# Kernel optimization log

Hardware: AMD Instinct MI355X
Metric: run time of the kernel (lower is better)

## Reference

```python
import jax, jax.numpy as jnp
import numpy as np

N_HEAD, D_K, D_V, EPS = 8, 64, 64, 1e-6


def setup_inputs() -> dict:
    key = jax.random.key(0)
    ks = jax.random.split(key, 7)
    b, n, t, d = 8, 4, 512, 512
    q = jax.random.normal(ks[0], (b, n, t, d), dtype=jnp.float32)
    k = jax.random.normal(ks[1], (b, n, t, d), dtype=jnp.float32)
    v = jax.random.normal(ks[2], (b, n, t, d), dtype=jnp.float32)
    s = 1.0 / np.sqrt(d)
    w_q = jax.random.normal(ks[3], (N_HEAD * D_K, d), dtype=jnp.float32) * s
    w_k = jax.random.normal(ks[4], (N_HEAD * D_K, d), dtype=jnp.float32) * s
    w_v = jax.random.normal(ks[5], (N_HEAD * D_V, d), dtype=jnp.float32) * s
    w_fc = jax.random.normal(ks[6], (d, N_HEAD * D_V), dtype=jnp.float32) * s
    ln_gamma = jnp.ones((d,), dtype=jnp.float32)
    ln_beta = jnp.zeros((d,), dtype=jnp.float32)
    return {"q": q, "k": k, "v": v, "w_q": w_q, "w_k": w_k, "w_v": w_v,
            "w_fc": w_fc, "ln_gamma": ln_gamma, "ln_beta": ln_beta}


def reference(q, k, v, w_q, w_k, w_v, w_fc, ln_gamma, ln_beta):
    b, n, t, d = q.shape
    B = b * n
    qf = q.reshape(B, t, d)
    kf = k.reshape(B, t, d)
    vf = v.reshape(B, t, d)
    residual = qf
    # projections -> [B, H, T, dk/dv]
    Q = jnp.einsum('btd,ed->bte', qf, w_q).reshape(B, t, N_HEAD, D_K).transpose(0, 2, 1, 3)
    K = jnp.einsum('btd,ed->bte', kf, w_k).reshape(B, t, N_HEAD, D_K).transpose(0, 2, 1, 3)
    V = jnp.einsum('btd,ed->bte', vf, w_v).reshape(B, t, N_HEAD, D_V).transpose(0, 2, 1, 3)
    # scaled dot-product attention (scale by sqrt(d_k) of q's last dim)
    scale = 1.0 / jnp.sqrt(jnp.asarray(D_K, dtype=Q.dtype))
    attn = jax.nn.softmax(jnp.einsum('bhqd,bhkd->bhqk', Q * scale, K), axis=-1)
    O = jnp.einsum('bhqk,bhkd->bhqd', attn, V)  # [B, H, T, dv]
    # merge heads, then the original's extra transpose+view (layout scramble)
    x = O.transpose(0, 2, 1, 3).reshape(B, t, N_HEAD * D_V)
    x = jnp.transpose(x, (0, 2, 1)).reshape(B, t, N_HEAD * D_V)
    x = jnp.einsum('bte,de->btd', x, w_fc)
    x = x + residual
    # LayerNorm(eps=1e-6)
    mu = jnp.mean(x, axis=-1, keepdims=True)
    var = jnp.var(x, axis=-1, keepdims=True)
    x = (x - mu) * jax.lax.rsqrt(var + EPS) * ln_gamma + ln_beta
    return x.reshape(b, n, t, d)
```

## Files before the change

kernel.cpp:

```cpp
#include <hip/hip_runtime.h>
#include <hip/hip_bf16.h>
#include <stdint.h>

typedef __attribute__((ext_vector_type(8))) short bf16x8;
typedef __attribute__((ext_vector_type(4))) float f32x4;
typedef unsigned int u32;

#define MFMA16(a,b,c) __builtin_amdgcn_mfma_f32_16x16x32_bf16((a),(b),(c),0,0,0)

__device__ __forceinline__ unsigned short f2bf(float f) {
    unsigned u = __float_as_uint(f);
    u = (u + 0x7FFFu + ((u >> 16) & 1u)) >> 16;
    return (unsigned short)u;
}
__device__ __forceinline__ float bf2f(unsigned short h) {
    return __uint_as_float(((unsigned)h) << 16);
}
__device__ __forceinline__ void gload16(const unsigned short* gp, unsigned short* lp) {
    __builtin_amdgcn_global_load_lds(
        (const __attribute__((address_space(1))) u32*)gp,
        (__attribute__((address_space(3))) u32*)lp, 16, 0, 0);
}
__device__ __forceinline__ int xcd_swz(int bid, int q8) {
    return (bid & 7) * q8 + (bid >> 3);
}


__global__ __launch_bounds__(256) void prep_kernel(
    const float* __restrict__ q, const float* __restrict__ k, const float* __restrict__ v,
    const float* __restrict__ wq, const float* __restrict__ wk, const float* __restrict__ wv,
    const float* __restrict__ wfc,
    unsigned short* __restrict__ Xq, unsigned short* __restrict__ Xk, unsigned short* __restrict__ Xv,
    unsigned short* __restrict__ Wcat)
{
    const long c = (long)blockIdx.x * 256 + threadIdx.x;
    const float* src;
    unsigned short* dst;
    long off;
    if (c < 3145728) {
        const int t = (int)(c >> 20);
        off = (c & 1048575) * 8;
        src = (t == 0) ? q : (t == 1) ? k : v;
        dst = (t == 0) ? Xq : (t == 1) ? Xk : Xv;
    } else {
        const long c2 = c - 3145728;
        const int w = (int)(c2 >> 15);
        off = (c2 & 32767) * 8;
        src = (w == 0) ? wq : (w == 1) ? wk : (w == 2) ? wv : wfc;
        dst = Wcat + (long)w * 262144;
    }
    const float4 a = *(const float4*)(src + off);
    const float4 b = *(const float4*)(src + off + 4);
    uint4 pk;
    pk.x = (u32)f2bf(a.x) | ((u32)f2bf(a.y) << 16);
    pk.y = (u32)f2bf(a.z) | ((u32)f2bf(a.w) << 16);
    pk.z = (u32)f2bf(b.x) | ((u32)f2bf(b.y) << 16);
    pk.w = (u32)f2bf(b.z) | ((u32)f2bf(b.w) << 16);
    *(uint4*)(dst + off) = pk;
}

__device__ __forceinline__ void gemm_body(
    const unsigned short* __restrict__ A, const unsigned short* __restrict__ Bm,
    unsigned short* __restrict__ out, int mode, float scale,
    unsigned short* As0, unsigned short* Bs0,
    unsigned short* As1, unsigned short* Bs1,
    int m0, int n0)
{
    const int tid = threadIdx.x, wid = tid >> 6, lane = tid & 63;
    const int wm = wid >> 1, wn = wid & 1;
    const int g = lane >> 4, cc = lane & 15;

    f32x4 acc[4][4];
    #pragma unroll
    for (int a = 0; a < 4; a++)
        #pragma unroll
        for (int b = 0; b < 4; b++)
            acc[a][b] = (f32x4){0.f, 0.f, 0.f, 0.f};

    auto STAGE = [&](unsigned short* As, unsigned short* Bs, int k0) {
        #pragma unroll
        for (int j = 0; j < 4; j++) {
            const int sb = j * 256 + wid * 64;
            const int s = sb + lane;
            const int r = s >> 3;
            const int cd = (s & 7) ^ (r & 7);
            gload16(A  + (size_t)(m0 + r) * 512 + k0 + cd * 8, As + (size_t)sb * 8);
            gload16(Bm + (size_t)(n0 + r) * 512 + k0 + cd * 8, Bs + (size_t)sb * 8);
        }
    };

    STAGE(As0, Bs0, 0);
    __syncthreads();

    #pragma unroll
    for (int t = 0; t < 8; t++) {
        unsigned short* Ac = (t & 1) ? As1 : As0;
        unsigned short* Bc = (t & 1) ? Bs1 : Bs0;
        if (t < 7)
            STAGE((t & 1) ? As0 : As1, (t & 1) ? Bs0 : Bs1, (t + 1) * 64);

        #pragma unroll
        for (int kc = 0; kc < 2; kc++) {
            bf16x8 af[4], bfr[4];
            #pragma unroll
            for (int mf = 0; mf < 4; mf++) {
                const int r = wm * 64 + mf * 16 + cc;
                af[mf] = *(const bf16x8*)(Ac + r * 64 + (((kc * 4 + g) ^ (r & 7)) * 8));
            }
            #pragma unroll
            for (int nf = 0; nf < 4; nf++) {
                const int r = wn * 64 + nf * 16 + cc;
                bfr[nf] = *(const bf16x8*)(Bc + r * 64 + (((kc * 4 + g) ^ (r & 7)) * 8));
            }
            __builtin_amdgcn_s_setprio(1);
            #pragma unroll
            for (int mf = 0; mf < 4; mf++)
                #pragma unroll
                for (int nf = 0; nf < 4; nf++)
                    acc[mf][nf] = MFMA16(af[mf], bfr[nf], acc[mf][nf]);
            __builtin_amdgcn_s_setprio(0);
        }
        __syncthreads();
    }

    #pragma unroll
    for (int mf = 0; mf < 4; mf++) {
        const int rg = m0 + wm * 64 + mf * 16 + g * 4;
        const int t0 = rg & 511, bI = rg >> 9;
        #pragma unroll
        for (int nf = 0; nf < 4; nf++) {
            const int col = n0 + wn * 64 + nf * 16 + cc;
            if (mode == 0) {
                const int h = col >> 6, dd = col & 63;
                const size_t base = ((size_t)((bI * 8 + h) * 512 + t0)) * 64 + dd;
                #pragma unroll
                for (int i = 0; i < 4; i++)
                    out[base + (size_t)i * 64] = f2bf(acc[mf][nf][i] * scale);
            } else if (mode == 1) {
                const int h = col >> 6, dd = col & 63;
                const size_t base = ((size_t)((bI * 8 + h) * 64 + dd)) * 512 + t0;
                uint2 pk;
                pk.x = (u32)f2bf(acc[mf][nf][0]) | ((u32)f2bf(acc[mf][nf][1]) << 16);
                pk.y = (u32)f2bf(acc[mf][nf][2]) | ((u32)f2bf(acc[mf][nf][3]) << 16);
                *(uint2*)(out + base) = pk;
            } else {
                #pragma unroll
                for (int i = 0; i < 4; i++)
                    out[(size_t)(rg + i) * 512 + col] = f2bf(acc[mf][nf][i]);
            }
        }
    }
}

__global__ __launch_bounds__(256) void proj_kernel(
    const unsigned short* __restrict__ Xq, const unsigned short* __restrict__ Xk,
    const unsigned short* __restrict__ Xv, const unsigned short* __restrict__ Wcat,
    unsigned short* __restrict__ Qb, unsigned short* __restrict__ Kb,
    unsigned short* __restrict__ Vt)
{
    __shared__ __align__(16) unsigned short As[2][128 * 64];
    __shared__ __align__(16) unsigned short Bs[2][128 * 64];
    const int work = xcd_swz(blockIdx.x, 192);
    const int x = work & 3, y = (work >> 2) & 127, z = work >> 9;
    const unsigned short* A = (z == 0) ? Xq : (z == 1) ? Xk : Xv;
    const unsigned short* B = Wcat + (size_t)z * 262144;
    unsigned short* out = (z == 0) ? Qb : (z == 1) ? Kb : Vt;
    const int mode = (z == 2) ? 1 : 0;
    const float scale = (z == 0) ? 0.125f : 1.0f;
    gemm_body(A, B, out, mode, scale, As[0], Bs[0], As[1], Bs[1], y * 128, x * 128);
}

__global__ __launch_bounds__(256) void fc_kernel(
    const unsigned short* __restrict__ Os, const unsigned short* __restrict__ Wfc,
    unsigned short* __restrict__ Y)
{
    __shared__ __align__(16) unsigned short As[2][128 * 64];
    __shared__ __align__(16) unsigned short Bs[2][128 * 64];
    const int work = xcd_swz(blockIdx.x, 64);
    const int x = work & 3, y = work >> 2;
    gemm_body(Os, Wfc, Y, 2, 1.0f, As[0], Bs[0], As[1], Bs[1], y * 128, x * 128);
}

__global__ __launch_bounds__(256) void attn_kernel(
    const unsigned short* __restrict__ Qb, const unsigned short* __restrict__ Kb,
    const unsigned short* __restrict__ Vt, unsigned short* __restrict__ Os)
{
    __shared__ __align__(16) unsigned short Ks[64 * 64];
    __shared__ __align__(16) unsigned short Vs[64 * 64];
    __shared__ __align__(16) unsigned short Ps[4 * 32 * 64];

    const int work = xcd_swz(blockIdx.x, 128);
    const int qt = work & 3, bh = work >> 2;
    const int tid = threadIdx.x;
    const int wid = tid >> 6, lane = tid & 63;
    const int g = lane >> 4, cc = lane & 15;

    const unsigned short* Qp = Qb + (size_t)bh * 512 * 64;
    const unsigned short* Kp = Kb + (size_t)bh * 512 * 64;
    const unsigned short* Vp = Vt + (size_t)bh * 64 * 512;

    const int q0 = qt * 128 + wid * 32;

    bf16x8 qf[2][2];
    #pragma unroll
    for (int mf = 0; mf < 2; mf++)
        #pragma unroll
        for (int kb = 0; kb < 2; kb++)
            qf[mf][kb] = *(const bf16x8*)(Qp + (size_t)(q0 + mf * 16 + cc) * 64 + kb * 32 + g * 8);

    f32x4 o[2][4];
    #pragma unroll
    for (int a = 0; a < 2; a++)
        #pragma unroll
        for (int b = 0; b < 4; b++)
            o[a][b] = (f32x4){0.f, 0.f, 0.f, 0.f};
    float lrun[2][4];
    #pragma unroll
    for (int a = 0; a < 2; a++)
        #pragma unroll
        for (int i = 0; i < 4; i++) lrun[a][i] = 0.f;

    const int sb = wid * 64;
    const int s1 = sb + lane, r1 = s1 >> 3, cd1 = (s1 & 7) ^ (r1 & 7);
    const int s2 = sb + 256 + lane, r2 = s2 >> 3, cd2 = (s2 & 7) ^ (r2 & 7);

    for (int kt = 0; kt < 8; kt++) {
        gload16(Kp + (size_t)(kt * 64 + r1) * 64 + cd1 * 8, Ks + (size_t)sb * 8);
        gload16(Kp + (size_t)(kt * 64 + r2) * 64 + cd2 * 8, Ks + (size_t)(sb + 256) * 8);
        gload16(Vp + (size_t)r1 * 512 + kt * 64 + cd1 * 8, Vs + (size_t)sb * 8);
        gload16(Vp + (size_t)r2 * 512 + kt * 64 + cd2 * 8, Vs + (size_t)(sb + 256) * 8);
        __syncthreads();

        f32x4 s[2][4];
        #pragma unroll
        for (int a = 0; a < 2; a++)
            #pragma unroll
            for (int b = 0; b < 4; b++)
                s[a][b] = (f32x4){0.f, 0.f, 0.f, 0.f};
        __builtin_amdgcn_s_setprio(1);
        #pragma unroll
        for (int nf = 0; nf < 4; nf++) {
            const int r = nf * 16 + cc;
            #pragma unroll
            for (int kb = 0; kb < 2; kb++) {
                bf16x8 kf = *(const bf16x8*)(Ks + r * 64 + (((kb * 4 + g) ^ (r & 7)) * 8));
                s[0][nf] = MFMA16(qf[0][kb], kf, s[0][nf]);
                s[1][nf] = MFMA16(qf[1][kb], kf, s[1][nf]);
            }
        }
        __builtin_amdgcn_s_setprio(0);

        unsigned short* Pw = Ps + wid * 32 * 64;
        #pragma unroll
        for (int mf = 0; mf < 2; mf++)
            #pragma unroll
            for (int i = 0; i < 4; i++) {
                float lacc = 0.f;
                #pragma unroll
                for (int nf = 0; nf < 4; nf++) {
                    float p = __expf(s[mf][nf][i]);
                    s[mf][nf][i] = p;
                    lacc += p;
                }
                lrun[mf][i] += lacc;
            }

        #pragma unroll
        for (int mf = 0; mf < 2; mf++)
            #pragma unroll
            for (int nf = 0; nf < 4; nf++) {
                const int c = nf * 16 + cc, csl = c >> 3, cin = c & 7;
                #pragma unroll
                for (int i = 0; i < 4; i++) {
                    const int row = mf * 16 + g * 4 + i;
                    Pw[row * 64 + ((csl ^ (row & 7)) * 8) + cin] = f2bf(s[mf][nf][i]);
                }
            }

        __builtin_amdgcn_s_setprio(1);
        #pragma unroll
        for (int kc = 0; kc < 2; kc++) {
            bf16x8 pa[2], vb[4];
            #pragma unroll
            for (int mf = 0; mf < 2; mf++) {
                const int r = mf * 16 + cc;
                pa[mf] = *(const bf16x8*)(Pw + r * 64 + (((kc * 4 + g) ^ (r & 7)) * 8));
            }
            #pragma unroll
            for (int vf = 0; vf < 4; vf++) {
                const int r = vf * 16 + cc;
                vb[vf] = *(const bf16x8*)(Vs + r * 64 + (((kc * 4 + g) ^ (r & 7)) * 8));
            }
            #pragma unroll
            for (int mf = 0; mf < 2; mf++)
                #pragma unroll
                for (int vf = 0; vf < 4; vf++)
                    o[mf][vf] = MFMA16(pa[mf], vb[vf], o[mf][vf]);
        }
        __builtin_amdgcn_s_setprio(0);
        __syncthreads();
    }

    const int b = bh >> 3, h = bh & 7;
    #pragma unroll
    for (int mf = 0; mf < 2; mf++) {
        int tq0 = q0 + mf * 16 + g * 4;
        float inv[4];
        #pragma unroll
        for (int i = 0; i < 4; i++) {
            float l = lrun[mf][i];
            #pragma unroll
            for (int d = 1; d < 16; d <<= 1) l += __shfl_xor(l, d);
            inv[i] = 1.0f / l;
        }
        #pragma unroll
        for (int vf = 0; vf < 4; vf++) {
            int dv = vf * 16 + cc;
            uint2 pk;
            pk.x = (u32)f2bf(o[mf][vf][0] * inv[0]) | ((u32)f2bf(o[mf][vf][1] * inv[1]) << 16);
            pk.y = (u32)f2bf(o[mf][vf][2] * inv[2]) | ((u32)f2bf(o[mf][vf][3] * inv[3]) << 16);
            size_t base = ((size_t)b * 512 + h * 64 + dv) * 512 + tq0;
            *(uint2*)(Os + base) = pk;
        }
    }
}

__global__ __launch_bounds__(256) void ln_kernel(
    const unsigned short* __restrict__ y, const float* __restrict__ resid,
    const float* __restrict__ gamma, const float* __restrict__ beta,
    float* __restrict__ out)
{
    const int wid = threadIdx.x >> 6, lane = threadIdx.x & 63;
    const int row = blockIdx.x * 4 + wid;
    const unsigned short* yr = y + (size_t)row * 512;
    const float* rr = resid + (size_t)row * 512;

    const bf16x8 yv = *(const bf16x8*)(yr + lane * 8);
    const float4 r0 = *(const float4*)(rr + lane * 8);
    const float4 r1 = *(const float4*)(rr + lane * 8 + 4);
    float x[8];
    x[0] = bf2f((unsigned short)yv[0]) + r0.x;
    x[1] = bf2f((unsigned short)yv[1]) + r0.y;
    x[2] = bf2f((unsigned short)yv[2]) + r0.z;
    x[3] = bf2f((unsigned short)yv[3]) + r0.w;
    x[4] = bf2f((unsigned short)yv[4]) + r1.x;
    x[5] = bf2f((unsigned short)yv[5]) + r1.y;
    x[6] = bf2f((unsigned short)yv[6]) + r1.z;
    x[7] = bf2f((unsigned short)yv[7]) + r1.w;

    float s = 0.f, sq = 0.f;
    #pragma unroll
    for (int j = 0; j < 8; j++) { s += x[j]; sq += x[j] * x[j]; }
    #pragma unroll
    for (int d = 1; d < 64; d <<= 1) {
        s += __shfl_xor(s, d);
        sq += __shfl_xor(sq, d);
    }
    const float mu = s * (1.0f / 512.0f);
    const float var = sq * (1.0f / 512.0f) - mu * mu;
    const float rs = rsqrtf(var + 1e-6f);

    #pragma unroll
    for (int j = 0; j < 2; j++) {
        const int colb = lane * 8 + j * 4;
        const float4 gg = *(const float4*)(gamma + colb);
        const float4 bb = *(const float4*)(beta + colb);
        float4 ov;
        ov.x = (x[j * 4 + 0] - mu) * rs * gg.x + bb.x;
        ov.y = (x[j * 4 + 1] - mu) * rs * gg.y + bb.y;
        ov.z = (x[j * 4 + 2] - mu) * rs * gg.z + bb.z;
        ov.w = (x[j * 4 + 3] - mu) * rs * gg.w + bb.w;
        *(float4*)(out + (size_t)row * 512 + colb) = ov;
    }
}

extern "C" void kernel_launch(void* const* d_in, const int* in_sizes, int n_in,
                              void* d_out, int out_size, void* d_ws, size_t ws_size,
                              hipStream_t stream) {
    const float* q     = (const float*)d_in[0];
    const float* k     = (const float*)d_in[1];
    const float* v     = (const float*)d_in[2];
    const float* wq    = (const float*)d_in[3];
    const float* wk    = (const float*)d_in[4];
    const float* wv    = (const float*)d_in[5];
    const float* wfc   = (const float*)d_in[6];
    const float* gamma = (const float*)d_in[7];
    const float* beta  = (const float*)d_in[8];
    float* out = (float*)d_out;

    char* ws = (char*)d_ws;
    const size_t SEG = 16777216;
    unsigned short* Xq   = (unsigned short*)(ws);
    unsigned short* Xk   = (unsigned short*)(ws + SEG);
    unsigned short* Xv   = (unsigned short*)(ws + 2 * SEG);
    unsigned short* Qb   = (unsigned short*)(ws + 3 * SEG);
    unsigned short* Kb   = (unsigned short*)(ws + 4 * SEG);
    unsigned short* Vt   = (unsigned short*)(ws + 5 * SEG);
    unsigned short* Wcat = (unsigned short*)(ws + 6 * SEG);
    unsigned short* Os = Xq;
    unsigned short* Y  = Xk;

    prep_kernel<<<12800, 256, 0, stream>>>(q, k, v, wq, wk, wv, wfc, Xq, Xk, Xv, Wcat);
    proj_kernel<<<1536, 256, 0, stream>>>(Xq, Xk, Xv, Wcat, Qb, Kb, Vt);
    attn_kernel<<<1024, 256, 0, stream>>>(Qb, Kb, Vt, Os);
    fc_kernel<<<512, 256, 0, stream>>>(Os, Wcat + 786432, Y);
    ln_kernel<<<4096, 256, 0, stream>>>(Y, q, gamma, beta, out);
}
```

Before: 128.1 us.

## Switch attention to 32x32 MFMA with in-register P transpose; read bf16 residual

```diff
diff --git a/kernel.cpp b/kernel.cpp
--- a/kernel.cpp
+++ b/kernel.cpp
@@ -4,9 +4,11 @@
 
 typedef __attribute__((ext_vector_type(8))) short bf16x8;
 typedef __attribute__((ext_vector_type(4))) float f32x4;
+typedef __attribute__((ext_vector_type(16))) float f32x16;
 typedef unsigned int u32;
 
 #define MFMA16(a,b,c) __builtin_amdgcn_mfma_f32_16x16x32_bf16((a),(b),(c),0,0,0)
+#define MFMA32(a,b,c) __builtin_amdgcn_mfma_f32_32x32x16_bf16((a),(b),(c),0,0,0)
 
 __device__ __forceinline__ unsigned short f2bf(float f) {
     unsigned u = __float_as_uint(f);
@@ -15,6 +17,11 @@
 }
 __device__ __forceinline__ float bf2f(unsigned short h) {
     return __uint_as_float(((unsigned)h) << 16);
+}
+__device__ __forceinline__ u32 cvt_pk_bf16(float lo, float hi) {
+    u32 r;
+    asm("v_cvt_pk_bf16_f32 %0, %1, %2" : "=v"(r) : "v"(lo), "v"(hi));
+    return r;
 }
 __device__ __forceinline__ void gload16(const unsigned short* gp, unsigned short* lp) {
     __builtin_amdgcn_global_load_lds(
@@ -187,13 +194,12 @@
 {
     __shared__ __align__(16) unsigned short Ks[64 * 64];
     __shared__ __align__(16) unsigned short Vs[64 * 64];
-    __shared__ __align__(16) unsigned short Ps[4 * 32 * 64];
 
     const int work = xcd_swz(blockIdx.x, 128);
     const int qt = work & 3, bh = work >> 2;
     const int tid = threadIdx.x;
     const int wid = tid >> 6, lane = tid & 63;
-    const int g = lane >> 4, cc = lane & 15;
+    const int l31 = lane & 31, hi = lane >> 5;
 
     const unsigned short* Qp = Qb + (size_t)bh * 512 * 64;
     const unsigned short* Kp = Kb + (size_t)bh * 512 * 64;
@@ -201,28 +207,21 @@
 
     const int q0 = qt * 128 + wid * 32;
 
-    bf16x8 qf[2][2];
-    #pragma unroll
-    for (int mf = 0; mf < 2; mf++)
-        #pragma unroll
-        for (int kb = 0; kb < 2; kb++)
-            qf[mf][kb] = *(const bf16x8*)(Qp + (size_t)(q0 + mf * 16 + cc) * 64 + kb * 32 + g * 8);
-
-    f32x4 o[2][4];
-    #pragma unroll
-    for (int a = 0; a < 2; a++)
-        #pragma unroll
-        for (int b = 0; b < 4; b++)
-            o[a][b] = (f32x4){0.f, 0.f, 0.f, 0.f};
-    float lrun[2][4];
-    #pragma unroll
-    for (int a = 0; a < 2; a++)
-        #pragma unroll
-        for (int i = 0; i < 4; i++) lrun[a][i] = 0.f;
+    bf16x8 qf[4];
+    #pragma unroll
+    for (int c = 0; c < 4; c++)
+        qf[c] = *(const bf16x8*)(Qp + (size_t)(q0 + l31) * 64 + c * 16 + hi * 8);
+
+    f32x16 o0, o1;
+    #pragma unroll
+    for (int r = 0; r < 16; r++) { o0[r] = 0.f; o1[r] = 0.f; }
+    float lrun = 0.f;
 
     const int sb = wid * 64;
     const int s1 = sb + lane, r1 = s1 >> 3, cd1 = (s1 & 7) ^ (r1 & 7);
     const int s2 = sb + 256 + lane, r2 = s2 >> 3, cd2 = (s2 & 7) ^ (r2 & 7);
+
+    const int swz0 = l31 & 7;
 
     for (int kt = 0; kt < 8; kt++) {
         gload16(Kp + (size_t)(kt * 64 + r1) * 64 + cd1 * 8, Ks + (size_t)sb * 8);
@@ -231,122 +230,92 @@
         gload16(Vp + (size_t)r2 * 512 + kt * 64 + cd2 * 8, Vs + (size_t)(sb + 256) * 8);
         __syncthreads();
 
-        f32x4 s[2][4];
-        #pragma unroll
-        for (int a = 0; a < 2; a++)
-            #pragma unroll
-            for (int b = 0; b < 4; b++)
-                s[a][b] = (f32x4){0.f, 0.f, 0.f, 0.f};
+        f32x16 sT0, sT1;
+        #pragma unroll
+        for (int r = 0; r < 16; r++) { sT0[r] = 0.f; sT1[r] = 0.f; }
         __builtin_amdgcn_s_setprio(1);
         #pragma unroll
-        for (int nf = 0; nf < 4; nf++) {
-            const int r = nf * 16 + cc;
-            #pragma unroll
-            for (int kb = 0; kb < 2; kb++) {
-                bf16x8 kf = *(const bf16x8*)(Ks + r * 64 + (((kb * 4 + g) ^ (r & 7)) * 8));
-                s[0][nf] = MFMA16(qf[0][kb], kf, s[0][nf]);
-                s[1][nf] = MFMA16(qf[1][kb], kf, s[1][nf]);
-            }
+        for (int c = 0; c < 4; c++) {
+            const int cs = c * 2 + hi;
+            bf16x8 kf0 = *(const bf16x8*)(Ks + l31 * 64 + ((cs ^ swz0) * 8));
+            bf16x8 kf1 = *(const bf16x8*)(Ks + (32 + l31) * 64 + ((cs ^ swz0) * 8));
+            sT0 = MFMA32(kf0, qf[c], sT0);
+            sT1 = MFMA32(kf1, qf[c], sT1);
         }
         __builtin_amdgcn_s_setprio(0);
 
-        unsigned short* Pw = Ps + wid * 32 * 64;
-        #pragma unroll
-        for (int mf = 0; mf < 2; mf++)
-            #pragma unroll
-            for (int i = 0; i < 4; i++) {
-                float lacc = 0.f;
-                #pragma unroll
-                for (int nf = 0; nf < 4; nf++) {
-                    float p = __expf(s[mf][nf][i]);
-                    s[mf][nf][i] = p;
-                    lacc += p;
-                }
-                lrun[mf][i] += lacc;
-            }
-
-        #pragma unroll
-        for (int mf = 0; mf < 2; mf++)
-            #pragma unroll
-            for (int nf = 0; nf < 4; nf++) {
-                const int c = nf * 16 + cc, csl = c >> 3, cin = c & 7;
-                #pragma unroll
-                for (int i = 0; i < 4; i++) {
-                    const int row = mf * 16 + g * 4 + i;
-                    Pw[row * 64 + ((csl ^ (row & 7)) * 8) + cin] = f2bf(s[mf][nf][i]);
-                }
-            }
+        u32 wA[8], xA[8], wB[8], xB[8];
+        #pragma unroll
+        for (int j = 0; j < 8; j++) {
+            float a0 = __expf(sT0[2 * j]), a1 = __expf(sT0[2 * j + 1]);
+            float b0 = __expf(sT1[2 * j]), b1 = __expf(sT1[2 * j + 1]);
+            lrun += (a0 + a1) + (b0 + b1);
+            wA[j] = cvt_pk_bf16(a0, a1);
+            wB[j] = cvt_pk_bf16(b0, b1);
+            xA[j] = __shfl_xor(wA[j], 32);
+            xB[j] = __shfl_xor(wB[j], 32);
+        }
 
         __builtin_amdgcn_s_setprio(1);
         #pragma unroll
-        for (int kc = 0; kc < 2; kc++) {
-            bf16x8 pa[2], vb[4];
-            #pragma unroll
-            for (int mf = 0; mf < 2; mf++) {
-                const int r = mf * 16 + cc;
-                pa[mf] = *(const bf16x8*)(Pw + r * 64 + (((kc * 4 + g) ^ (r & 7)) * 8));
-            }
-            #pragma unroll
-            for (int vf = 0; vf < 4; vf++) {
-                const int r = vf * 16 + cc;
-                vb[vf] = *(const bf16x8*)(Vs + r * 64 + (((kc * 4 + g) ^ (r & 7)) * 8));
-            }
-            #pragma unroll
-            for (int mf = 0; mf < 2; mf++)
-                #pragma unroll
-                for (int vf = 0; vf < 4; vf++)
-                    o[mf][vf] = MFMA16(pa[mf], vb[vf], o[mf][vf]);
+        for (int ck = 0; ck < 4; ck++) {
+            const u32* w = (ck < 2) ? wA : wB;
+            const u32* x = (ck < 2) ? xA : xB;
+            const int jb = (ck & 1) * 4;
+            union { u32 u[4]; bf16x8 v; } pa;
+            pa.u[0] = hi ? x[jb + 2] : w[jb + 0];
+            pa.u[1] = hi ? x[jb + 3] : w[jb + 1];
+            pa.u[2] = hi ? w[jb + 2] : x[jb + 0];
+            pa.u[3] = hi ? w[jb + 3] : x[jb + 1];
+            const int cs = ck * 2 + hi;
+            bf16x8 vb0 = *(const bf16x8*)(Vs + l31 * 64 + ((cs ^ swz0) * 8));
+            bf16x8 vb1 = *(const bf16x8*)(Vs + (32 + l31) * 64 + ((cs ^ swz0) * 8));
+            o0 = MFMA32(pa.v, vb0, o0);
+            o1 = MFMA32(pa.v, vb1, o1);
         }
         __builtin_amdgcn_s_setprio(0);
         __syncthreads();
     }
 
+    const float lsum = lrun + __shfl_xor(lrun, 32);
+    const float inv = 1.0f / lsum;
+    float iv[16];
+    #pragma unroll
+    for (int qd = 0; qd < 4; qd++)
+        #pragma unroll
+        for (int i = 0; i < 4; i++)
+            iv[qd * 4 + i] = __shfl(inv, qd * 8 + 4 * hi + i);
+
     const int b = bh >> 3, h = bh & 7;
     #pragma unroll
-    for (int mf = 0; mf < 2; mf++) {
-        int tq0 = q0 + mf * 16 + g * 4;
-        float inv[4];
-        #pragma unroll
-        for (int i = 0; i < 4; i++) {
-            float l = lrun[mf][i];
-            #pragma unroll
-            for (int d = 1; d < 16; d <<= 1) l += __shfl_xor(l, d);
-            inv[i] = 1.0f / l;
-        }
-        #pragma unroll
-        for (int vf = 0; vf < 4; vf++) {
-            int dv = vf * 16 + cc;
+    for (int dvt = 0; dvt < 2; dvt++) {
+        const f32x16& o = dvt ? o1 : o0;
+        const int dv = dvt * 32 + l31;
+        const size_t rowbase = ((size_t)b * 512 + h * 64 + dv) * 512;
+        #pragma unroll
+        for (int qd = 0; qd < 4; qd++) {
             uint2 pk;
-            pk.x = (u32)f2bf(o[mf][vf][0] * inv[0]) | ((u32)f2bf(o[mf][vf][1] * inv[1]) << 16);
-            pk.y = (u32)f2bf(o[mf][vf][2] * inv[2]) | ((u32)f2bf(o[mf][vf][3] * inv[3]) << 16);
-            size_t base = ((size_t)b * 512 + h * 64 + dv) * 512 + tq0;
-            *(uint2*)(Os + base) = pk;
+            pk.x = cvt_pk_bf16(o[qd * 4 + 0] * iv[qd * 4 + 0], o[qd * 4 + 1] * iv[qd * 4 + 1]);
+            pk.y = cvt_pk_bf16(o[qd * 4 + 2] * iv[qd * 4 + 2], o[qd * 4 + 3] * iv[qd * 4 + 3]);
+            *(uint2*)(Os + rowbase + q0 + qd * 8 + 4 * hi) = pk;
         }
     }
 }
 
 __global__ __launch_bounds__(256) void ln_kernel(
-    const unsigned short* __restrict__ y, const float* __restrict__ resid,
+    const unsigned short* __restrict__ y, const unsigned short* __restrict__ residb,
     const float* __restrict__ gamma, const float* __restrict__ beta,
     float* __restrict__ out)
 {
     const int wid = threadIdx.x >> 6, lane = threadIdx.x & 63;
     const int row = blockIdx.x * 4 + wid;
-    const unsigned short* yr = y + (size_t)row * 512;
-    const float* rr = resid + (size_t)row * 512;
-
-    const bf16x8 yv = *(const bf16x8*)(yr + lane * 8);
-    const float4 r0 = *(const float4*)(rr + lane * 8);
-    const float4 r1 = *(const float4*)(rr + lane * 8 + 4);
+
+    const bf16x8 yv = *(const bf16x8*)(y + (size_t)row * 512 + lane * 8);
+    const bf16x8 rv = *(const bf16x8*)(residb + (size_t)row * 512 + lane * 8);
     float x[8];
-    x[0] = bf2f((unsigned short)yv[0]) + r0.x;
-    x[1] = bf2f((unsigned short)yv[1]) + r0.y;
-    x[2] = bf2f((unsigned short)yv[2]) + r0.z;
-    x[3] = bf2f((unsigned short)yv[3]) + r0.w;
-    x[4] = bf2f((unsigned short)yv[4]) + r1.x;
-    x[5] = bf2f((unsigned short)yv[5]) + r1.y;
-    x[6] = bf2f((unsigned short)yv[6]) + r1.z;
-    x[7] = bf2f((unsigned short)yv[7]) + r1.w;
+    #pragma unroll
+    for (int j = 0; j < 8; j++)
+        x[j] = bf2f((unsigned short)yv[j]) + bf2f((unsigned short)rv[j]);
 
     float s = 0.f, sq = 0.f;
     #pragma unroll
@@ -397,12 +366,12 @@
     unsigned short* Kb   = (unsigned short*)(ws + 4 * SEG);
     unsigned short* Vt   = (unsigned short*)(ws + 5 * SEG);
     unsigned short* Wcat = (unsigned short*)(ws + 6 * SEG);
-    unsigned short* Os = Xq;
+    unsigned short* Os = Xv;
     unsigned short* Y  = Xk;
 
     prep_kernel<<<12800, 256, 0, stream>>>(q, k, v, wq, wk, wv, wfc, Xq, Xk, Xv, Wcat);
     proj_kernel<<<1536, 256, 0, stream>>>(Xq, Xk, Xv, Wcat, Qb, Kb, Vt);
     attn_kernel<<<1024, 256, 0, stream>>>(Qb, Kb, Vt, Os);
     fc_kernel<<<512, 256, 0, stream>>>(Os, Wcat + 786432, Y);
-    ln_kernel<<<4096, 256, 0, stream>>>(Y, q, gamma, beta, out);
-}
+    ln_kernel<<<4096, 256, 0, stream>>>(Y, Xq, gamma, beta, out);
+}
```

New measurement: 122.3 us. -4.6%, faster.
